# Optimization experiments

Measured on AMD Instinct MI355X. Metric: run time of the kernel, lower is better.

The kernel has to match this reference:

```python
import jax, jax.numpy as jnp
import numpy as np
from jax import lax


def setup_inputs() -> dict:
    key = jax.random.key(0)
    I = jax.random.uniform(key, (32, 3, 512, 512), dtype=jnp.float32)
    return {"I": I, "k": 15}


def reference(I, k):
    # Channel-wise min -> dark channel (torch does this via -max_pool over transposed channel dim)
    dark = jnp.min(I, axis=1, keepdims=True)  # [B,1,H,W]
    p = k // 2
    # Spatial min-pool kxk, stride 1, pad k//2. torch max_pool2d pads with -inf,
    # so the min-pool equivalent pads with +inf: reduce_window with min and +inf init.
    eroded = lax.reduce_window(
        dark,
        jnp.inf,
        lax.min,
        window_dimensions=(1, 1, k, k),
        window_strides=(1, 1, 1, 1),
        padding=[(0, 0), (0, 0), (p, p), (p, p)],
    )
    return eroded
```

## Files before the change

kernel.cpp:

```cpp
#include <hip/hip_runtime.h>
#include <math.h>

#define BATCH 32
#define CH    3
#define H     512
#define W     512
#define KWIN  15
#define PAD   7
#define T2    16

static __device__ __forceinline__ float2 min2(float2 a, float2 b) {
    float2 r;
    r.x = fminf(a.x, b.x);
    r.y = fminf(a.y, b.y);
    return r;
}
static __device__ __forceinline__ float4 min4(float4 a, float4 b) {
    float4 r;
    r.x = fminf(a.x, b.x); r.y = fminf(a.y, b.y);
    r.z = fminf(a.z, b.z); r.w = fminf(a.w, b.w);
    return r;
}

__global__ void dcp_p1(const float* __restrict__ I, float* __restrict__ tmp) {
    const int wid = (blockIdx.x << 2) + (threadIdx.x >> 6);
    const int b   = wid >> 9;
    const int h   = wid & (H - 1);
    const int L   = threadIdx.x & 63;
    const int x   = L * 8;

    const float* p = I + ((size_t)b * CH * H + h) * W + x;
    const float4 a0 = *(const float4*)(p);
    const float4 a1 = *(const float4*)(p + 4);
    const float4 b0 = *(const float4*)(p + (size_t)H * W);
    const float4 b1 = *(const float4*)(p + (size_t)H * W + 4);
    const float4 c0 = *(const float4*)(p + (size_t)2 * H * W);
    const float4 c1 = *(const float4*)(p + (size_t)2 * H * W + 4);

    const float4 mlo = min4(min4(a0, b0), c0);
    const float4 mhi = min4(min4(a1, b1), c1);
    const float m0 = mlo.x, m1 = mlo.y, m2 = mlo.z, m3 = mlo.w;
    const float m4 = mhi.x, m5 = mhi.y, m6 = mhi.z, m7 = mhi.w;

    float pr[8], sf[8];
    pr[0] = m0; pr[1] = fminf(pr[0], m1); pr[2] = fminf(pr[1], m2);
    pr[3] = fminf(pr[2], m3); pr[4] = fminf(pr[3], m4); pr[5] = fminf(pr[4], m5);
    pr[6] = fminf(pr[5], m6); pr[7] = fminf(pr[6], m7);
    sf[7] = m7; sf[6] = fminf(m6, sf[7]); sf[5] = fminf(m5, sf[6]);
    sf[4] = fminf(m4, sf[5]); sf[3] = fminf(m3, sf[4]); sf[2] = fminf(m2, sf[3]);
    sf[1] = fminf(m1, sf[2]); sf[0] = fminf(m0, sf[1]);
    const float M = pr[7];

    float sl[7], pn[7];
    #pragma unroll
    for (int j = 0; j < 7; ++j) {
        sl[j] = __shfl_up(sf[j + 1], 1);
        pn[j] = __shfl_down(pr[j], 1);
    }
    if (L == 0) {
        #pragma unroll
        for (int j = 0; j < 7; ++j) sl[j] = INFINITY;
    }
    if (L == 63) {
        #pragma unroll
        for (int j = 0; j < 7; ++j) pn[j] = INFINITY;
    }

    float4 olo, ohi;
    olo.x = fminf(M, sl[0]);
    olo.y = fminf(M, fminf(sl[1], pn[0]));
    olo.z = fminf(M, fminf(sl[2], pn[1]));
    olo.w = fminf(M, fminf(sl[3], pn[2]));
    ohi.x = fminf(M, fminf(sl[4], pn[3]));
    ohi.y = fminf(M, fminf(sl[5], pn[4]));
    ohi.z = fminf(M, fminf(sl[6], pn[5]));
    ohi.w = fminf(M, pn[6]);

    float* q = tmp + ((size_t)b * H + h) * W + x;
    *(float4*)(q)     = olo;
    *(float4*)(q + 4) = ohi;
}

__global__ void dcp_p2(const float* __restrict__ tmp, float* __restrict__ out) {
    const int x  = threadIdx.x * 2;
    const int y0 = blockIdx.x * T2;
    const int b  = blockIdx.y;

    const float* col = tmp + (size_t)b * H * W + x;
    float*       o   = out + (size_t)b * H * W + x;

    float2 vb[KWIN];
    #pragma unroll
    for (int j = 0; j < KWIN; ++j) {
        const int y = min(y0 + 8 + j, H - 1);
        vb[j] = *(const float2*)(col + (size_t)y * W);
    }
    if (y0 + 8 + KWIN - 1 >= H) {
        const float2 inf2 = make_float2(INFINITY, INFINITY);
        #pragma unroll
        for (int j = 0; j < KWIN; ++j)
            if (y0 + 8 + j >= H) vb[j] = inf2;
    }
    float2 P[KWIN];
    P[0] = vb[0];
    #pragma unroll
    for (int j = 1; j < KWIN; ++j) P[j] = min2(P[j - 1], vb[j]);
    *(float2*)(o + (size_t)(y0 + 15) * W) = P[14];

    float2 va[KWIN];
    #pragma unroll
    for (int i = 0; i < KWIN; ++i) {
        const int y = max(y0 - PAD + i, 0);
        va[i] = *(const float2*)(col + (size_t)y * W);
    }
    if (y0 == 0) {
        const float2 inf2 = make_float2(INFINITY, INFINITY);
        #pragma unroll
        for (int i = 0; i < PAD; ++i) va[i] = inf2;
    }
    float2 run = va[14];
    *(float2*)(o + (size_t)(y0 + 14) * W) = min2(run, P[13]);
    #pragma unroll
    for (int r = 13; r >= 1; --r) {
        run = min2(run, va[r]);
        *(float2*)(o + (size_t)(y0 + r) * W) = min2(run, P[r - 1]);
    }
    run = min2(run, va[0]);
    *(float2*)(o + (size_t)y0 * W) = run;
}

extern "C" void kernel_launch(void* const* d_in, const int* in_sizes, int n_in,
                              void* d_out, int out_size, void* d_ws, size_t ws_size,
                              hipStream_t stream) {
    const float* I = (const float*)d_in[0];
    float* out = (float*)d_out;
    float* tmp = (float*)d_ws;

    dcp_p1<<<dim3((BATCH * H) / 4), dim3(256), 0, stream>>>(I, tmp);
    dcp_p2<<<dim3(H / T2, BATCH), dim3(256), 0, stream>>>(tmp, out);
}
```

Measured before the change: 167.4 us.

## Fuse channel-min/horizontal pass and vertical min pass via shared memory tile

Merges the two kernels into one: each block computes horizontally eroded dark-channel rows for its 16-row tile plus halo into LDS, then performs the vertical 15-row min from LDS. This removes the intermediate global tmp buffer write/read and a kernel launch. In exchange each block recomputes halo rows, so input reads rise by the halo ratio, and the large LDS tile limits occupancy.

```diff
diff --git a/kernel.cpp b/kernel.cpp
--- a/kernel.cpp
+++ b/kernel.cpp
@@ -7,7 +7,8 @@
 #define W     512
 #define KWIN  15
 #define PAD   7
-#define T2    16
+#define TH    16
+#define NR    (TH + KWIN - 1)
 
 static __device__ __forceinline__ float2 min2(float2 a, float2 b) {
     float2 r;
@@ -22,111 +23,101 @@
     return r;
 }
 
-__global__ void dcp_p1(const float* __restrict__ I, float* __restrict__ tmp) {
-    const int wid = (blockIdx.x << 2) + (threadIdx.x >> 6);
-    const int b   = wid >> 9;
-    const int h   = wid & (H - 1);
-    const int L   = threadIdx.x & 63;
-    const int x   = L * 8;
+__global__ void dcp_fused5(const float* __restrict__ I, float* __restrict__ out) {
+    const int b    = blockIdx.y;
+    const int y0   = blockIdx.x * TH;
+    const int tid  = threadIdx.x;
+    const int wave = tid >> 6;
+    const int L    = tid & 63;
+    const int x    = L * 8;
 
-    const float* p = I + ((size_t)b * CH * H + h) * W + x;
-    const float4 a0 = *(const float4*)(p);
-    const float4 a1 = *(const float4*)(p + 4);
-    const float4 b0 = *(const float4*)(p + (size_t)H * W);
-    const float4 b1 = *(const float4*)(p + (size_t)H * W + 4);
-    const float4 c0 = *(const float4*)(p + (size_t)2 * H * W);
-    const float4 c1 = *(const float4*)(p + (size_t)2 * H * W + 4);
+    __shared__ float hm[NR][W];
 
-    const float4 mlo = min4(min4(a0, b0), c0);
-    const float4 mhi = min4(min4(a1, b1), c1);
-    const float m0 = mlo.x, m1 = mlo.y, m2 = mlo.z, m3 = mlo.w;
-    const float m4 = mhi.x, m5 = mhi.y, m6 = mhi.z, m7 = mhi.w;
+    const float* base = I + (size_t)b * CH * H * W;
 
-    float pr[8], sf[8];
-    pr[0] = m0; pr[1] = fminf(pr[0], m1); pr[2] = fminf(pr[1], m2);
-    pr[3] = fminf(pr[2], m3); pr[4] = fminf(pr[3], m4); pr[5] = fminf(pr[4], m5);
-    pr[6] = fminf(pr[5], m6); pr[7] = fminf(pr[6], m7);
-    sf[7] = m7; sf[6] = fminf(m6, sf[7]); sf[5] = fminf(m5, sf[6]);
-    sf[4] = fminf(m4, sf[5]); sf[3] = fminf(m3, sf[4]); sf[2] = fminf(m2, sf[3]);
-    sf[1] = fminf(m1, sf[2]); sf[0] = fminf(m0, sf[1]);
-    const float M = pr[7];
+    #pragma unroll
+    for (int ii = 0; ii < (NR + 3) / 4; ++ii) {
+        const int i = wave + ii * 4;
+        if (i < NR) {
+            const int y  = y0 - PAD + i;
+            const int yc = min(max(y, 0), H - 1);
+            const float* p = base + (size_t)yc * W + x;
+            const float4 a0 = *(const float4*)(p);
+            const float4 a1 = *(const float4*)(p + 4);
+            const float4 b0 = *(const float4*)(p + (size_t)H * W);
+            const float4 b1 = *(const float4*)(p + (size_t)H * W + 4);
+            const float4 c0 = *(const float4*)(p + (size_t)2 * H * W);
+            const float4 c1 = *(const float4*)(p + (size_t)2 * H * W + 4);
+            float4 mlo = min4(min4(a0, b0), c0);
+            float4 mhi = min4(min4(a1, b1), c1);
+            if (y < 0 || y >= H) {
+                mlo = make_float4(INFINITY, INFINITY, INFINITY, INFINITY);
+                mhi = mlo;
+            }
+            const float m0 = mlo.x, m1 = mlo.y, m2 = mlo.z, m3 = mlo.w;
+            const float m4 = mhi.x, m5 = mhi.y, m6 = mhi.z, m7 = mhi.w;
 
-    float sl[7], pn[7];
+            float pr[8], sf[8];
+            pr[0] = m0;            pr[1] = fminf(pr[0], m1);
+            pr[2] = fminf(pr[1], m2); pr[3] = fminf(pr[2], m3);
+            pr[4] = fminf(pr[3], m4); pr[5] = fminf(pr[4], m5);
+            pr[6] = fminf(pr[5], m6); pr[7] = fminf(pr[6], m7);
+            sf[7] = m7;            sf[6] = fminf(m6, sf[7]);
+            sf[5] = fminf(m5, sf[6]); sf[4] = fminf(m4, sf[5]);
+            sf[3] = fminf(m3, sf[4]); sf[2] = fminf(m2, sf[3]);
+            sf[1] = fminf(m1, sf[2]); sf[0] = fminf(m0, sf[1]);
+            const float M = pr[7];
+
+            float sl[7], pn[7];
+            #pragma unroll
+            for (int j = 0; j < 7; ++j) {
+                sl[j] = __shfl_up(sf[j + 1], 1);
+                pn[j] = __shfl_down(pr[j], 1);
+            }
+            if (L == 0) {
+                #pragma unroll
+                for (int j = 0; j < 7; ++j) sl[j] = INFINITY;
+            }
+            if (L == 63) {
+                #pragma unroll
+                for (int j = 0; j < 7; ++j) pn[j] = INFINITY;
+            }
+
+            float4 olo, ohi;
+            olo.x = fminf(M, sl[0]);
+            olo.y = fminf(M, fminf(sl[1], pn[0]));
+            olo.z = fminf(M, fminf(sl[2], pn[1]));
+            olo.w = fminf(M, fminf(sl[3], pn[2]));
+            ohi.x = fminf(M, fminf(sl[4], pn[3]));
+            ohi.y = fminf(M, fminf(sl[5], pn[4]));
+            ohi.z = fminf(M, fminf(sl[6], pn[5]));
+            ohi.w = fminf(M, pn[6]);
+
+            *(float4*)&hm[i][x]     = olo;
+            *(float4*)&hm[i][x + 4] = ohi;
+        }
+    }
+    __syncthreads();
+
+    const int xc = tid * 2;
+    float*    o  = out + ((size_t)b * H + y0) * W + xc;
+
+    float2 P[KWIN];
+    P[0] = *(const float2*)&hm[KWIN][xc];
     #pragma unroll
-    for (int j = 0; j < 7; ++j) {
-        sl[j] = __shfl_up(sf[j + 1], 1);
-        pn[j] = __shfl_down(pr[j], 1);
-    }
-    if (L == 0) {
-        #pragma unroll
-        for (int j = 0; j < 7; ++j) sl[j] = INFINITY;
-    }
-    if (L == 63) {
-        #pragma unroll
-        for (int j = 0; j < 7; ++j) pn[j] = INFINITY;
-    }
+    for (int j = 1; j < KWIN; ++j)
+        P[j] = min2(P[j - 1], *(const float2*)&hm[KWIN + j][xc]);
+    *(float2*)(o + (size_t)15 * W) = P[14];
 
-    float4 olo, ohi;
-    olo.x = fminf(M, sl[0]);
-    olo.y = fminf(M, fminf(sl[1], pn[0]));
-    olo.z = fminf(M, fminf(sl[2], pn[1]));
-    olo.w = fminf(M, fminf(sl[3], pn[2]));
-    ohi.x = fminf(M, fminf(sl[4], pn[3]));
-    ohi.y = fminf(M, fminf(sl[5], pn[4]));
-    ohi.z = fminf(M, fminf(sl[6], pn[5]));
-    ohi.w = fminf(M, pn[6]);
-
-    float* q = tmp + ((size_t)b * H + h) * W + x;
-    *(float4*)(q)     = olo;
-    *(float4*)(q + 4) = ohi;
-}
-
-__global__ void dcp_p2(const float* __restrict__ tmp, float* __restrict__ out) {
-    const int x  = threadIdx.x * 2;
-    const int y0 = blockIdx.x * T2;
-    const int b  = blockIdx.y;
-
-    const float* col = tmp + (size_t)b * H * W + x;
-    float*       o   = out + (size_t)b * H * W + x;
-
-    float2 vb[KWIN];
-    #pragma unroll
-    for (int j = 0; j < KWIN; ++j) {
-        const int y = min(y0 + 8 + j, H - 1);
-        vb[j] = *(const float2*)(col + (size_t)y * W);
-    }
-    if (y0 + 8 + KWIN - 1 >= H) {
-        const float2 inf2 = make_float2(INFINITY, INFINITY);
-        #pragma unroll
-        for (int j = 0; j < KWIN; ++j)
-            if (y0 + 8 + j >= H) vb[j] = inf2;
-    }
-    float2 P[KWIN];
-    P[0] = vb[0];
-    #pragma unroll
-    for (int j = 1; j < KWIN; ++j) P[j] = min2(P[j - 1], vb[j]);
-    *(float2*)(o + (size_t)(y0 + 15) * W) = P[14];
-
-    float2 va[KWIN];
-    #pragma unroll
-    for (int i = 0; i < KWIN; ++i) {
-        const int y = max(y0 - PAD + i, 0);
-        va[i] = *(const float2*)(col + (size_t)y * W);
-    }
-    if (y0 == 0) {
-        const float2 inf2 = make_float2(INFINITY, INFINITY);
-        #pragma unroll
-        for (int i = 0; i < PAD; ++i) va[i] = inf2;
-    }
-    float2 run = va[14];
-    *(float2*)(o + (size_t)(y0 + 14) * W) = min2(run, P[13]);
+    float2 run = *(const float2*)&hm[14][xc];
+    *(float2*)(o + (size_t)14 * W) = min2(run, P[13]);
     #pragma unroll
     for (int r = 13; r >= 1; --r) {
-        run = min2(run, va[r]);
-        *(float2*)(o + (size_t)(y0 + r) * W) = min2(run, P[r - 1]);
+        run = min2(run, *(const float2*)&hm[r][xc]);
+        *(float2*)(o + (size_t)r * W) = min2(run, P[r - 1]);
     }
-    run = min2(run, va[0]);
-    *(float2*)(o + (size_t)y0 * W) = run;
+    run = min2(run, *(const float2*)&hm[0][xc]);
+    *(float2*)(o) = run;
 }
 
 extern "C" void kernel_launch(void* const* d_in, const int* in_sizes, int n_in,
@@ -134,8 +125,5 @@
                               hipStream_t stream) {
     const float* I = (const float*)d_in[0];
     float* out = (float*)d_out;
-    float* tmp = (float*)d_ws;
-
-    dcp_p1<<<dim3((BATCH * H) / 4), dim3(256), 0, stream>>>(I, tmp);
-    dcp_p2<<<dim3(H / T2, BATCH), dim3(256), 0, stream>>>(tmp, out);
+    dcp_fused5<<<dim3(H / TH, BATCH), dim3(256), 0, stream>>>(I, out);
 }
```

Measured after the change: 163.7 us. -2.2%, faster.
